# Kernel tuning notes

Hardware: AMD Instinct MI355X
Metric: run time of the kernel (lower is better)

Reference implementation:

```python
import jax, jax.numpy as jnp
import numpy as np

EMBED_DIM = 256
NUM_HEADS = 8
WINDOW = 64
HEAD_DIM = EMBED_DIM // NUM_HEADS


def setup_inputs() -> dict:
    key = jax.random.key(0)
    k_x, k_w, k_ow = jax.random.split(key, 3)
    B, S, E = 2, 4096, EMBED_DIM
    x = jax.random.normal(k_x, (B, S, E), dtype=jnp.float32)
    # nn.MultiheadAttention params: packed in_proj (q,k,v) and out_proj
    bound = 1.0 / np.sqrt(E)
    in_proj_w = jax.random.uniform(k_w, (3 * E, E), jnp.float32, -bound, bound)
    in_proj_b = jnp.zeros((3 * E,), jnp.float32)
    out_w = jax.random.uniform(k_ow, (E, E), jnp.float32, -bound, bound)
    out_b = jnp.zeros((E,), jnp.float32)
    return {"x": x, "in_proj_w": in_proj_w, "in_proj_b": in_proj_b,
            "out_w": out_w, "out_b": out_b}


def reference(x, in_proj_w, in_proj_b, out_w, out_b):
    B, S, E = x.shape
    H, D = NUM_HEADS, HEAD_DIM
    # packed qkv projection (torch Linear: y = x @ W^T + b)
    qkv = jnp.einsum('bse,fe->bsf', x, in_proj_w) + in_proj_b  # [B,S,3E]
    q, k, v = jnp.split(qkv, 3, axis=-1)
    q = q.reshape(B, S, H, D).transpose(0, 2, 1, 3)  # [B,H,S,D]
    k = k.reshape(B, S, H, D).transpose(0, 2, 1, 3)
    v = v.reshape(B, S, H, D).transpose(0, 2, 1, 3)
    scale = 1.0 / jnp.sqrt(jnp.asarray(D, x.dtype))
    scores = jnp.einsum('bhqd,bhkd->bhqk', q * scale, k)  # [B,H,S,S]
    idx = jnp.arange(S)
    band = jnp.abs(idx[:, None] - idx[None, :]) <= WINDOW  # [S,S]
    neg = jnp.asarray(-1e9, scores.dtype)
    scores = jnp.where(band[None, None, :, :], scores, neg)
    attn = jax.nn.softmax(scores, axis=-1)
    out = jnp.einsum('bhqk,bhkd->bhqd', attn, v)  # [B,H,S,D]
    out = out.transpose(0, 2, 1, 3).reshape(B, S, E)
    return jnp.einsum('bse,fe->bsf', out, out_w) + out_b
```

## Files before the change

### kernel.cpp

```cpp
#include <hip/hip_runtime.h>
#include <hip/hip_bf16.h>

#define S_LEN 4096
#define EMB   256
#define NHEAD 8
#define HDIM  32
#define WIN   64
#define BATCH 2

typedef __attribute__((ext_vector_type(8))) short short8;
typedef __attribute__((ext_vector_type(4))) float floatx4;
typedef unsigned short u16;
typedef unsigned int   u32;

static __device__ __forceinline__ u32 bf16_rn(float x) {
    u32 u = __float_as_uint(x);
    return (u + 0x7FFFu + ((u >> 16) & 1u)) >> 16;
}
static __device__ __forceinline__ u32 packsplit(float x) {
    const u32 hi = bf16_rn(x);
    const float hf = __uint_as_float(hi << 16);
    const u32 lo = bf16_rn(x - hf);
    return (hi << 16) | lo;
}
static __device__ __forceinline__ void unpack_pair(u32 p0, u32 p1, u32& h, u32& l) {
    h = (p0 >> 16) | (p1 & 0xFFFF0000u);
    l = (p0 & 0xFFFFu) | (p1 << 16);
}
static __device__ __forceinline__ void unpack8(uint4 a, uint4 b, uint4& h, uint4& l) {
    unpack_pair(a.x, a.y, h.x, l.x);
    unpack_pair(a.z, a.w, h.y, l.y);
    unpack_pair(b.x, b.y, h.z, l.z);
    unpack_pair(b.z, b.w, h.w, l.w);
}

#define NX4 524288
#define NW4 49152
#define NO4 16384

__global__ __launch_bounds__(256) void convert_kernel(
    const float* __restrict__ X, const float* __restrict__ Wi, const float* __restrict__ Wo,
    u32* __restrict__ Xp, u32* __restrict__ Wip, u32* __restrict__ Wop)
{
    const int i = blockIdx.x * 256 + threadIdx.x;
    const float* src; u32* dst; int off;
    if (i < NX4)            { src = X;  dst = Xp;  off = i; }
    else if (i < NX4 + NW4) { src = Wi; dst = Wip; off = i - NX4; }
    else                    { src = Wo; dst = Wop; off = i - NX4 - NW4; }
    const float4 v = *(const float4*)(src + (size_t)off * 4);
    uint4 o;
    o.x = packsplit(v.x); o.y = packsplit(v.y);
    o.z = packsplit(v.z); o.w = packsplit(v.w);
    *(uint4*)(dst + (size_t)off * 4) = o;
}

#define LDA 40

__global__ __launch_bounds__(256) void qkv_proj_kernel(
    const u32* __restrict__ Xp, const u32* __restrict__ Wp,
    const float* __restrict__ bias,
    u32* __restrict__ Qp, u32* __restrict__ Kp, u32* __restrict__ Vp)
{
    __shared__ __align__(16) u16 Ah[128 * LDA], Al[128 * LDA];
    __shared__ __align__(16) u16 Bh[64 * LDA],  Bl[64 * LDA];
    const int tid = threadIdx.x;
    const int m0 = blockIdx.y * 128, n0 = blockIdx.x * 64;
    const int srow = tid >> 2, sc = tid & 3;
    const int lane = tid & 63, wv = tid >> 6;
    const int wm = (wv >> 1) * 64, wn = (wv & 1) * 32;
    const int lm = lane & 15, kq = lane >> 4;

    uint4 pA[2][2], pB[2];
#pragma unroll
    for (int r = 0; r < 2; ++r) {
        const u32* base = Xp + (size_t)(m0 + srow + r * 64) * EMB + sc * 8;
        pA[r][0] = *(const uint4*)base;
        pA[r][1] = *(const uint4*)(base + 4);
    }
    {
        const u32* base = Wp + (size_t)(n0 + srow) * EMB + sc * 8;
        pB[0] = *(const uint4*)base;
        pB[1] = *(const uint4*)(base + 4);
    }

    floatx4 acc[4][2] = {};
    for (int t = 0; t < 8; ++t) {
        __syncthreads();
#pragma unroll
        for (int r = 0; r < 2; ++r) {
            uint4 h, l;
            unpack8(pA[r][0], pA[r][1], h, l);
            *(uint4*)&Ah[(srow + r * 64) * LDA + sc * 8] = h;
            *(uint4*)&Al[(srow + r * 64) * LDA + sc * 8] = l;
        }
        {
            uint4 h, l;
            unpack8(pB[0], pB[1], h, l);
            *(uint4*)&Bh[srow * LDA + sc * 8] = h;
            *(uint4*)&Bl[srow * LDA + sc * 8] = l;
        }
        __syncthreads();
        if (t < 7) {
            const int k0 = (t + 1) * 32;
#pragma unroll
            for (int r = 0; r < 2; ++r) {
                const u32* base = Xp + (size_t)(m0 + srow + r * 64) * EMB + k0 + sc * 8;
                pA[r][0] = *(const uint4*)base;
                pA[r][1] = *(const uint4*)(base + 4);
            }
            const u32* base = Wp + (size_t)(n0 + srow) * EMB + k0 + sc * 8;
            pB[0] = *(const uint4*)base;
            pB[1] = *(const uint4*)(base + 4);
        }
        short8 a_h[4], a_l[4], b_h[2], b_l[2];
#pragma unroll
        for (int mt = 0; mt < 4; ++mt) {
            a_h[mt] = *(const short8*)&Ah[(wm + mt * 16 + lm) * LDA + kq * 8];
            a_l[mt] = *(const short8*)&Al[(wm + mt * 16 + lm) * LDA + kq * 8];
        }
#pragma unroll
        for (int nt = 0; nt < 2; ++nt) {
            b_h[nt] = *(const short8*)&Bh[(wn + nt * 16 + lm) * LDA + kq * 8];
            b_l[nt] = *(const short8*)&Bl[(wn + nt * 16 + lm) * LDA + kq * 8];
        }
#pragma unroll
        for (int mt = 0; mt < 4; ++mt)
#pragma unroll
            for (int nt = 0; nt < 2; ++nt) {
                acc[mt][nt] = __builtin_amdgcn_mfma_f32_16x16x32_bf16(a_h[mt], b_h[nt], acc[mt][nt], 0, 0, 0);
                acc[mt][nt] = __builtin_amdgcn_mfma_f32_16x16x32_bf16(a_h[mt], b_l[nt], acc[mt][nt], 0, 0, 0);
                acc[mt][nt] = __builtin_amdgcn_mfma_f32_16x16x32_bf16(a_l[mt], b_h[nt], acc[mt][nt], 0, 0, 0);
            }
    }
#pragma unroll
    for (int nt = 0; nt < 2; ++nt) {
        const int f = n0 + wn + nt * 16 + lm;
        const int which = f >> 8;
        const int h = (f & 255) >> 5, d = f & 31;
        u32* dst = (which == 0) ? Qp : ((which == 1) ? Kp : Vp);
        const float sc2 = (which == 0) ? 0.17677669529663687f : 1.0f;
        const float bf = bias[f];
#pragma unroll
        for (int mt = 0; mt < 4; ++mt)
#pragma unroll
            for (int r = 0; r < 4; ++r) {
                const int m = m0 + wm + mt * 16 + kq * 4 + r;
                const int b = m >> 12, s = m & (S_LEN - 1);
                dst[(((size_t)b * NHEAD + h) * S_LEN + s) * HDIM + d]
                    = packsplit((acc[mt][nt][r] + bf) * sc2);
            }
    }
}

__global__ __launch_bounds__(256) void out_proj_kernel(
    const u32* __restrict__ Abp, const u32* __restrict__ Wp,
    const float* __restrict__ bias, float* __restrict__ C)
{
    __shared__ __align__(16) u16 Ah[128 * LDA], Al[128 * LDA];
    __shared__ __align__(16) u16 Bh[64 * LDA],  Bl[64 * LDA];
    const int tid = threadIdx.x;
    const int m0 = blockIdx.y * 128, n0 = blockIdx.x * 64;
    const int srow = tid >> 2, sc = tid & 3;
    const int lane = tid & 63, wv = tid >> 6;
    const int wm = (wv >> 1) * 64, wn = (wv & 1) * 32;
    const int lm = lane & 15, kq = lane >> 4;

    uint4 pA[2][2], pB[2];
#pragma unroll
    for (int r = 0; r < 2; ++r) {
        const u32* base = Abp + (size_t)(m0 + srow + r * 64) * EMB + sc * 8;
        pA[r][0] = *(const uint4*)base;
        pA[r][1] = *(const uint4*)(base + 4);
    }
    {
        const u32* base = Wp + (size_t)(n0 + srow) * EMB + sc * 8;
        pB[0] = *(const uint4*)base;
        pB[1] = *(const uint4*)(base + 4);
    }

    floatx4 acc[4][2] = {};
    for (int t = 0; t < 8; ++t) {
        __syncthreads();
#pragma unroll
        for (int r = 0; r < 2; ++r) {
            uint4 h, l;
            unpack8(pA[r][0], pA[r][1], h, l);
            *(uint4*)&Ah[(srow + r * 64) * LDA + sc * 8] = h;
            *(uint4*)&Al[(srow + r * 64) * LDA + sc * 8] = l;
        }
        {
            uint4 h, l;
            unpack8(pB[0], pB[1], h, l);
            *(uint4*)&Bh[srow * LDA + sc * 8] = h;
            *(uint4*)&Bl[srow * LDA + sc * 8] = l;
        }
        __syncthreads();
        if (t < 7) {
            const int k0 = (t + 1) * 32;
#pragma unroll
            for (int r = 0; r < 2; ++r) {
                const u32* base = Abp + (size_t)(m0 + srow + r * 64) * EMB + k0 + sc * 8;
                pA[r][0] = *(const uint4*)base;
                pA[r][1] = *(const uint4*)(base + 4);
            }
            const u32* base = Wp + (size_t)(n0 + srow) * EMB + k0 + sc * 8;
            pB[0] = *(const uint4*)base;
            pB[1] = *(const uint4*)(base + 4);
        }
        short8 a_h[4], a_l[4], b_h[2], b_l[2];
#pragma unroll
        for (int mt = 0; mt < 4; ++mt) {
            a_h[mt] = *(const short8*)&Ah[(wm + mt * 16 + lm) * LDA + kq * 8];
            a_l[mt] = *(const short8*)&Al[(wm + mt * 16 + lm) * LDA + kq * 8];
        }
#pragma unroll
        for (int nt = 0; nt < 2; ++nt) {
            b_h[nt] = *(const short8*)&Bh[(wn + nt * 16 + lm) * LDA + kq * 8];
            b_l[nt] = *(const short8*)&Bl[(wn + nt * 16 + lm) * LDA + kq * 8];
        }
#pragma unroll
        for (int mt = 0; mt < 4; ++mt)
#pragma unroll
            for (int nt = 0; nt < 2; ++nt) {
                acc[mt][nt] = __builtin_amdgcn_mfma_f32_16x16x32_bf16(a_h[mt], b_h[nt], acc[mt][nt], 0, 0, 0);
                acc[mt][nt] = __builtin_amdgcn_mfma_f32_16x16x32_bf16(a_h[mt], b_l[nt], acc[mt][nt], 0, 0, 0);
                acc[mt][nt] = __builtin_amdgcn_mfma_f32_16x16x32_bf16(a_l[mt], b_h[nt], acc[mt][nt], 0, 0, 0);
            }
    }
#pragma unroll
    for (int nt = 0; nt < 2; ++nt) {
        const int f = n0 + wn + nt * 16 + lm;
        const float bf = bias[f];
#pragma unroll
        for (int mt = 0; mt < 4; ++mt)
#pragma unroll
            for (int r = 0; r < 4; ++r) {
                const int m = m0 + wm + mt * 16 + kq * 4 + r;
                C[(size_t)m * EMB + f] = acc[mt][nt][r] + bf;
            }
    }
}

#define AKS 40
#define AVS 200
#define APS 200

__global__ __launch_bounds__(256) void local_attn_kernel(
    const u32* __restrict__ Qp, const u32* __restrict__ Kp,
    const u32* __restrict__ Vp, u32* __restrict__ Abp)
{
    __shared__ __align__(16) u16 Qh[64 * AKS], Ql[64 * AKS];
    __shared__ __align__(16) u16 Kh[192 * AKS], Kl[192 * AKS];
    __shared__ __align__(16) u16 Vt[32 * AVS];
    __shared__ __align__(16) u16 Pw[4 * 16 * APS];

    const int tid = threadIdx.x;
    const int q0 = blockIdx.x * 64;
    const int h = blockIdx.y, b = blockIdx.z;
    const int jmin = max(0, q0 - WIN);
    const int jmax = min(S_LEN - 1, q0 + 63 + WIN);
    const int nk = jmax - jmin + 1;
    const size_t bhS = ((size_t)b * NHEAD + h) * S_LEN;
    const size_t qoff = (bhS + q0) * HDIM;
    const size_t koff = (bhS + jmin) * HDIM;

    const int srow = tid >> 2, sc = tid & 3;
    {
        const u32* base = Qp + qoff + (size_t)srow * HDIM + sc * 8;
        uint4 h4, l4;
        unpack8(*(const uint4*)base, *(const uint4*)(base + 4), h4, l4);
        *(uint4*)&Qh[srow * AKS + sc * 8] = h4;
        *(uint4*)&Ql[srow * AKS + sc * 8] = l4;
    }
#pragma unroll
    for (int r = 0; r < 3; ++r) {
        const int t = srow + r * 64;
        const int tc = min(t, nk - 1);
        const u32* base = Kp + koff + (size_t)tc * HDIM + sc * 8;
        uint4 h4, l4;
        unpack8(*(const uint4*)base, *(const uint4*)(base + 4), h4, l4);
        *(uint4*)&Kh[t * AKS + sc * 8] = h4;
        *(uint4*)&Kl[t * AKS + sc * 8] = l4;
    }
#pragma unroll
    for (int r = 0; r < 3; ++r) {
        const int t = srow + r * 64;
        const int tc = min(t, nk - 1);
        const u32* base = Vp + koff + (size_t)tc * HDIM + sc * 8;
        const uint4 v0 = *(const uint4*)base;
        const uint4 v1 = *(const uint4*)(base + 4);
        const int d0 = sc * 8;
        Vt[(d0 + 0) * AVS + t] = (u16)(v0.x >> 16);
        Vt[(d0 + 1) * AVS + t] = (u16)(v0.y >> 16);
        Vt[(d0 + 2) * AVS + t] = (u16)(v0.z >> 16);
        Vt[(d0 + 3) * AVS + t] = (u16)(v0.w >> 16);
        Vt[(d0 + 4) * AVS + t] = (u16)(v1.x >> 16);
        Vt[(d0 + 5) * AVS + t] = (u16)(v1.y >> 16);
        Vt[(d0 + 6) * AVS + t] = (u16)(v1.z >> 16);
        Vt[(d0 + 7) * AVS + t] = (u16)(v1.w >> 16);
    }
    __syncthreads();

    const int lane = tid & 63, wv = tid >> 6;
    const int lm = lane & 15, quad = lane >> 4;
    const int qbase = wv * 16;

    const short8 qh = *(const short8*)&Qh[(qbase + lm) * AKS + quad * 8];
    const short8 ql = *(const short8*)&Ql[(qbase + lm) * AKS + quad * 8];

    floatx4 sacc[12];
#pragma unroll
    for (int nt = 0; nt < 12; ++nt) {
        const short8 bh = *(const short8*)&Kh[(nt * 16 + lm) * AKS + quad * 8];
        const short8 bl = *(const short8*)&Kl[(nt * 16 + lm) * AKS + quad * 8];
        floatx4 a = {};
        a = __builtin_amdgcn_mfma_f32_16x16x32_bf16(qh, bh, a, 0, 0, 0);
        a = __builtin_amdgcn_mfma_f32_16x16x32_bf16(qh, bl, a, 0, 0, 0);
        a = __builtin_amdgcn_mfma_f32_16x16x32_bf16(ql, bh, a, 0, 0, 0);
        sacc[nt] = a;
    }

    const int qg = q0 + qbase + quad * 4;
    float mx[4] = {-1e30f, -1e30f, -1e30f, -1e30f};
#pragma unroll
    for (int nt = 0; nt < 12; ++nt) {
        const int slot = nt * 16 + lm;
        const int keyg = jmin + slot;
#pragma unroll
        for (int r = 0; r < 4; ++r) {
            const int qr = qg + r;
            const bool valid = (slot < nk) && (keyg >= qr - WIN) && (keyg <= qr + WIN);
            const float sv = valid ? sacc[nt][r] : -1e30f;
            sacc[nt][r] = sv;
            mx[r] = fmaxf(mx[r], sv);
        }
    }
#pragma unroll
    for (int r = 0; r < 4; ++r) {
        mx[r] = fmaxf(mx[r], __shfl_xor(mx[r], 1));
        mx[r] = fmaxf(mx[r], __shfl_xor(mx[r], 2));
        mx[r] = fmaxf(mx[r], __shfl_xor(mx[r], 4));
        mx[r] = fmaxf(mx[r], __shfl_xor(mx[r], 8));
    }
    float l[4] = {0.f, 0.f, 0.f, 0.f};
    u16* Pme = &Pw[wv * 16 * APS];
#pragma unroll
    for (int nt = 0; nt < 12; ++nt)
#pragma unroll
        for (int r = 0; r < 4; ++r) {
            const float p = __expf(sacc[nt][r] - mx[r]);
            l[r] += p;
            Pme[(quad * 4 + r) * APS + nt * 16 + lm] = (u16)bf16_rn(p);
        }
#pragma unroll
    for (int r = 0; r < 4; ++r) {
        l[r] += __shfl_xor(l[r], 1);
        l[r] += __shfl_xor(l[r], 2);
        l[r] += __shfl_xor(l[r], 4);
        l[r] += __shfl_xor(l[r], 8);
    }
    const float rl[4] = {1.f / l[0], 1.f / l[1], 1.f / l[2], 1.f / l[3]};

    floatx4 oacc[2] = {};
#pragma unroll
    for (int ks = 0; ks < 6; ++ks) {
        const short8 ap  = *(const short8*)&Pme[lm * APS + ks * 32 + quad * 8];
        const short8 bv0 = *(const short8*)&Vt[lm * AVS + ks * 32 + quad * 8];
        const short8 bv1 = *(const short8*)&Vt[(16 + lm) * AVS + ks * 32 + quad * 8];
        oacc[0] = __builtin_amdgcn_mfma_f32_16x16x32_bf16(ap, bv0, oacc[0], 0, 0, 0);
        oacc[1] = __builtin_amdgcn_mfma_f32_16x16x32_bf16(ap, bv1, oacc[1], 0, 0, 0);
    }
#pragma unroll
    for (int nt = 0; nt < 2; ++nt)
#pragma unroll
        for (int r = 0; r < 4; ++r) {
            const int qrow = qbase + quad * 4 + r;
            Abp[((size_t)b * S_LEN + q0 + qrow) * EMB + h * HDIM + nt * 16 + lm]
                = packsplit(oacc[nt][r] * rl[r]);
        }
}

extern "C" void kernel_launch(void* const* d_in, const int* in_sizes, int n_in,
                              void* d_out, int out_size, void* d_ws, size_t ws_size,
                              hipStream_t stream) {
    const float* x  = (const float*)d_in[0];
    const float* wi = (const float*)d_in[1];
    const float* bi = (const float*)d_in[2];
    const float* wo = (const float*)d_in[3];
    const float* bo = (const float*)d_in[4];
    float* out = (float*)d_out;

    const size_t per = (size_t)BATCH * NHEAD * S_LEN * HDIM;
    u32* p = (u32*)d_ws;
    u32* Xp  = p; p += per;
    u32* Wip = p; p += 768 * EMB;
    u32* Wop = p; p += EMB * EMB;
    u32* Qp  = p; p += per;
    u32* Kp  = p; p += per;
    u32* Vp  = p; p += per;
    u32* Abp = p; p += per;

    convert_kernel<<<dim3((NX4 + NW4 + NO4) / 256), 256, 0, stream>>>(
        x, wi, wo, Xp, Wip, Wop);
    qkv_proj_kernel<<<dim3(768 / 64, 8192 / 128), 256, 0, stream>>>(
        Xp, Wip, bi, Qp, Kp, Vp);
    local_attn_kernel<<<dim3(S_LEN / 64, NHEAD, BATCH), 256, 0, stream>>>(
        Qp, Kp, Vp, Abp);
    out_proj_kernel<<<dim3(256 / 64, 8192 / 128), 256, 0, stream>>>(
        Abp, Wop, bo, out);
}
```

Measured before the change: 115.1 us.

## Compute transposed scores in registers and skip empty key tiles in local attention

The attention kernel now computes S^T (key-major) so each lane holds one query's scores. Q is loaded straight into registers and P is packed into MFMA A-operands without the shared-memory round trip. Each wave processes only the 10 key tiles that can overlap its band instead of all 12, which cuts MFMA work and LDS traffic. The output projection tile is also halved to 64 rows, doubling the grid to raise occupancy and parallelism, at the cost of less operand reuse per block.

```diff
diff --git a/kernel.cpp b/kernel.cpp
--- a/kernel.cpp
+++ b/kernel.cpp
@@ -156,21 +156,20 @@
     const u32* __restrict__ Abp, const u32* __restrict__ Wp,
     const float* __restrict__ bias, float* __restrict__ C)
 {
-    __shared__ __align__(16) u16 Ah[128 * LDA], Al[128 * LDA];
-    __shared__ __align__(16) u16 Bh[64 * LDA],  Bl[64 * LDA];
+    __shared__ __align__(16) u16 Ah[64 * LDA], Al[64 * LDA];
+    __shared__ __align__(16) u16 Bh[64 * LDA], Bl[64 * LDA];
     const int tid = threadIdx.x;
-    const int m0 = blockIdx.y * 128, n0 = blockIdx.x * 64;
+    const int m0 = blockIdx.y * 64, n0 = blockIdx.x * 64;
     const int srow = tid >> 2, sc = tid & 3;
     const int lane = tid & 63, wv = tid >> 6;
-    const int wm = (wv >> 1) * 64, wn = (wv & 1) * 32;
+    const int wm = (wv >> 1) * 32, wn = (wv & 1) * 32;
     const int lm = lane & 15, kq = lane >> 4;
 
-    uint4 pA[2][2], pB[2];
-#pragma unroll
-    for (int r = 0; r < 2; ++r) {
-        const u32* base = Abp + (size_t)(m0 + srow + r * 64) * EMB + sc * 8;
-        pA[r][0] = *(const uint4*)base;
-        pA[r][1] = *(const uint4*)(base + 4);
+    uint4 pA[2], pB[2];
+    {
+        const u32* base = Abp + (size_t)(m0 + srow) * EMB + sc * 8;
+        pA[0] = *(const uint4*)base;
+        pA[1] = *(const uint4*)(base + 4);
     }
     {
         const u32* base = Wp + (size_t)(n0 + srow) * EMB + sc * 8;
@@ -178,15 +177,14 @@
         pB[1] = *(const uint4*)(base + 4);
     }
 
-    floatx4 acc[4][2] = {};
+    floatx4 acc[2][2] = {};
     for (int t = 0; t < 8; ++t) {
         __syncthreads();
-#pragma unroll
-        for (int r = 0; r < 2; ++r) {
+        {
             uint4 h, l;
-            unpack8(pA[r][0], pA[r][1], h, l);
-            *(uint4*)&Ah[(srow + r * 64) * LDA + sc * 8] = h;
-            *(uint4*)&Al[(srow + r * 64) * LDA + sc * 8] = l;
+            unpack8(pA[0], pA[1], h, l);
+            *(uint4*)&Ah[srow * LDA + sc * 8] = h;
+            *(uint4*)&Al[srow * LDA + sc * 8] = l;
         }
         {
             uint4 h, l;
@@ -197,19 +195,18 @@
         __syncthreads();
         if (t < 7) {
             const int k0 = (t + 1) * 32;
-#pragma unroll
-            for (int r = 0; r < 2; ++r) {
-                const u32* base = Abp + (size_t)(m0 + srow + r * 64) * EMB + k0 + sc * 8;
-                pA[r][0] = *(const uint4*)base;
-                pA[r][1] = *(const uint4*)(base + 4);
+            {
+                const u32* base = Abp + (size_t)(m0 + srow) * EMB + k0 + sc * 8;
+                pA[0] = *(const uint4*)base;
+                pA[1] = *(const uint4*)(base + 4);
             }
             const u32* base = Wp + (size_t)(n0 + srow) * EMB + k0 + sc * 8;
             pB[0] = *(const uint4*)base;
             pB[1] = *(const uint4*)(base + 4);
         }
-        short8 a_h[4], a_l[4], b_h[2], b_l[2];
-#pragma unroll
-        for (int mt = 0; mt < 4; ++mt) {
+        short8 a_h[2], a_l[2], b_h[2], b_l[2];
+#pragma unroll
+        for (int mt = 0; mt < 2; ++mt) {
             a_h[mt] = *(const short8*)&Ah[(wm + mt * 16 + lm) * LDA + kq * 8];
             a_l[mt] = *(const short8*)&Al[(wm + mt * 16 + lm) * LDA + kq * 8];
         }
@@ -219,7 +216,7 @@
             b_l[nt] = *(const short8*)&Bl[(wn + nt * 16 + lm) * LDA + kq * 8];
         }
 #pragma unroll
-        for (int mt = 0; mt < 4; ++mt)
+        for (int mt = 0; mt < 2; ++mt)
 #pragma unroll
             for (int nt = 0; nt < 2; ++nt) {
                 acc[mt][nt] = __builtin_amdgcn_mfma_f32_16x16x32_bf16(a_h[mt], b_h[nt], acc[mt][nt], 0, 0, 0);
@@ -232,7 +229,7 @@
         const int f = n0 + wn + nt * 16 + lm;
         const float bf = bias[f];
 #pragma unroll
-        for (int mt = 0; mt < 4; ++mt)
+        for (int mt = 0; mt < 2; ++mt)
 #pragma unroll
             for (int r = 0; r < 4; ++r) {
                 const int m = m0 + wm + mt * 16 + kq * 4 + r;
@@ -243,16 +240,13 @@
 
 #define AKS 40
 #define AVS 200
-#define APS 200
 
 __global__ __launch_bounds__(256) void local_attn_kernel(
     const u32* __restrict__ Qp, const u32* __restrict__ Kp,
     const u32* __restrict__ Vp, u32* __restrict__ Abp)
 {
-    __shared__ __align__(16) u16 Qh[64 * AKS], Ql[64 * AKS];
     __shared__ __align__(16) u16 Kh[192 * AKS], Kl[192 * AKS];
     __shared__ __align__(16) u16 Vt[32 * AVS];
-    __shared__ __align__(16) u16 Pw[4 * 16 * APS];
 
     const int tid = threadIdx.x;
     const int q0 = blockIdx.x * 64;
@@ -264,14 +258,15 @@
     const size_t qoff = (bhS + q0) * HDIM;
     const size_t koff = (bhS + jmin) * HDIM;
 
+    const int lane = tid & 63, wv = tid >> 6;
+    const int lm = lane & 15, quad = lane >> 4;
+    const int qbase = wv * 16;
+
+    const u32* qb = Qp + qoff + (size_t)(qbase + lm) * HDIM + quad * 8;
+    const uint4 qp0 = *(const uint4*)qb;
+    const uint4 qp1 = *(const uint4*)(qb + 4);
+
     const int srow = tid >> 2, sc = tid & 3;
-    {
-        const u32* base = Qp + qoff + (size_t)srow * HDIM + sc * 8;
-        uint4 h4, l4;
-        unpack8(*(const uint4*)base, *(const uint4*)(base + 4), h4, l4);
-        *(uint4*)&Qh[srow * AKS + sc * 8] = h4;
-        *(uint4*)&Ql[srow * AKS + sc * 8] = l4;
-    }
 #pragma unroll
     for (int r = 0; r < 3; ++r) {
         const int t = srow + r * 64;
@@ -299,84 +294,100 @@
         Vt[(d0 + 6) * AVS + t] = (u16)(v1.z >> 16);
         Vt[(d0 + 7) * AVS + t] = (u16)(v1.w >> 16);
     }
+
+    short8 qh, ql;
+    {
+        uint4 h4, l4;
+        unpack8(qp0, qp1, h4, l4);
+        qh = *(const short8*)&h4;
+        ql = *(const short8*)&l4;
+    }
+
     __syncthreads();
 
-    const int lane = tid & 63, wv = tid >> 6;
-    const int lm = lane & 15, quad = lane >> 4;
-    const int qbase = wv * 16;
-
-    const short8 qh = *(const short8*)&Qh[(qbase + lm) * AKS + quad * 8];
-    const short8 ql = *(const short8*)&Ql[(qbase + lm) * AKS + quad * 8];
-
-    floatx4 sacc[12];
-#pragma unroll
-    for (int nt = 0; nt < 12; ++nt) {
-        const short8 bh = *(const short8*)&Kh[(nt * 16 + lm) * AKS + quad * 8];
-        const short8 bl = *(const short8*)&Kl[(nt * 16 + lm) * AKS + quad * 8];
+    const int tb = max(0, ((wv >> 1) << 1) + (min(q0 - WIN, 0) >> 4));
+
+    floatx4 sacc[10];
+#pragma unroll
+    for (int i = 0; i < 10; ++i) {
+        const int nt = tb + i;
+        const short8 kh = *(const short8*)&Kh[(nt * 16 + lm) * AKS + quad * 8];
+        const short8 kl = *(const short8*)&Kl[(nt * 16 + lm) * AKS + quad * 8];
         floatx4 a = {};
-        a = __builtin_amdgcn_mfma_f32_16x16x32_bf16(qh, bh, a, 0, 0, 0);
-        a = __builtin_amdgcn_mfma_f32_16x16x32_bf16(qh, bl, a, 0, 0, 0);
-        a = __builtin_amdgcn_mfma_f32_16x16x32_bf16(ql, bh, a, 0, 0, 0);
-        sacc[nt] = a;
-    }
-
-    const int qg = q0 + qbase + quad * 4;
-    float mx[4] = {-1e30f, -1e30f, -1e30f, -1e30f};
-#pragma unroll
-    for (int nt = 0; nt < 12; ++nt) {
-        const int slot = nt * 16 + lm;
-        const int keyg = jmin + slot;
+        a = __builtin_amdgcn_mfma_f32_16x16x32_bf16(kh, qh, a, 0, 0, 0);
+        a = __builtin_amdgcn_mfma_f32_16x16x32_bf16(kh, ql, a, 0, 0, 0);
+        a = __builtin_amdgcn_mfma_f32_16x16x32_bf16(kl, qh, a, 0, 0, 0);
+        sacc[i] = a;
+    }
+
+    const int qr = q0 + qbase + lm;
+    float mx = -1e30f;
+#pragma unroll
+    for (int i = 0; i < 10; ++i) {
+        const int sbase = (tb + i) * 16 + quad * 4;
 #pragma unroll
         for (int r = 0; r < 4; ++r) {
-            const int qr = qg + r;
+            const int slot = sbase + r;
+            const int keyg = jmin + slot;
             const bool valid = (slot < nk) && (keyg >= qr - WIN) && (keyg <= qr + WIN);
-            const float sv = valid ? sacc[nt][r] : -1e30f;
-            sacc[nt][r] = sv;
-            mx[r] = fmaxf(mx[r], sv);
-        }
-    }
-#pragma unroll
-    for (int r = 0; r < 4; ++r) {
-        mx[r] = fmaxf(mx[r], __shfl_xor(mx[r], 1));
-        mx[r] = fmaxf(mx[r], __shfl_xor(mx[r], 2));
-        mx[r] = fmaxf(mx[r], __shfl_xor(mx[r], 4));
-        mx[r] = fmaxf(mx[r], __shfl_xor(mx[r], 8));
-    }
-    float l[4] = {0.f, 0.f, 0.f, 0.f};
-    u16* Pme = &Pw[wv * 16 * APS];
-#pragma unroll
-    for (int nt = 0; nt < 12; ++nt)
-#pragma unroll
-        for (int r = 0; r < 4; ++r) {
-            const float p = __expf(sacc[nt][r] - mx[r]);
-            l[r] += p;
-            Pme[(quad * 4 + r) * APS + nt * 16 + lm] = (u16)bf16_rn(p);
-        }
-#pragma unroll
-    for (int r = 0; r < 4; ++r) {
-        l[r] += __shfl_xor(l[r], 1);
-        l[r] += __shfl_xor(l[r], 2);
-        l[r] += __shfl_xor(l[r], 4);
-        l[r] += __shfl_xor(l[r], 8);
-    }
-    const float rl[4] = {1.f / l[0], 1.f / l[1], 1.f / l[2], 1.f / l[3]};
-
+            const float sv = valid ? sacc[i][r] : -1e30f;
+            sacc[i][r] = sv;
+            mx = fmaxf(mx, sv);
+        }
+    }
+    mx = fmaxf(mx, __shfl_xor(mx, 16));
+    mx = fmaxf(mx, __shfl_xor(mx, 32));
+
+    float l = 0.f;
+    u32 pk_[20];
+#pragma unroll
+    for (int i = 0; i < 10; ++i) {
+        const float p0 = __expf(sacc[i][0] - mx);
+        const float p1 = __expf(sacc[i][1] - mx);
+        const float p2 = __expf(sacc[i][2] - mx);
+        const float p3 = __expf(sacc[i][3] - mx);
+        l += (p0 + p1) + (p2 + p3);
+        pk_[2 * i]     = bf16_rn(p0) | (bf16_rn(p1) << 16);
+        pk_[2 * i + 1] = bf16_rn(p2) | (bf16_rn(p3) << 16);
+    }
+    l += __shfl_xor(l, 16);
+    l += __shfl_xor(l, 32);
+    const float rl = 1.f / l;
+
+    const int kb = tb >> 1;
     floatx4 oacc[2] = {};
 #pragma unroll
-    for (int ks = 0; ks < 6; ++ks) {
-        const short8 ap  = *(const short8*)&Pme[lm * APS + ks * 32 + quad * 8];
-        const short8 bv0 = *(const short8*)&Vt[lm * AVS + ks * 32 + quad * 8];
-        const short8 bv1 = *(const short8*)&Vt[(16 + lm) * AVS + ks * 32 + quad * 8];
+    for (int i = 0; i < 5; ++i) {
+        const int ks = kb + i;
+        uint4 aw;
+        aw.x = pk_[4 * i + 0];
+        aw.y = pk_[4 * i + 1];
+        aw.z = pk_[4 * i + 2];
+        aw.w = pk_[4 * i + 3];
+        const short8 ap = *(const short8*)&aw;
+        const int sb = ks * 32 + quad * 4;
+        const uint2 e0 = *(const uint2*)&Vt[lm * AVS + sb];
+        const uint2 o0 = *(const uint2*)&Vt[lm * AVS + sb + 16];
+        const uint2 e1 = *(const uint2*)&Vt[(16 + lm) * AVS + sb];
+        const uint2 o1 = *(const uint2*)&Vt[(16 + lm) * AVS + sb + 16];
+        uint4 bw0; bw0.x = e0.x; bw0.y = e0.y; bw0.z = o0.x; bw0.w = o0.y;
+        uint4 bw1; bw1.x = e1.x; bw1.y = e1.y; bw1.z = o1.x; bw1.w = o1.y;
+        const short8 bv0 = *(const short8*)&bw0;
+        const short8 bv1 = *(const short8*)&bw1;
         oacc[0] = __builtin_amdgcn_mfma_f32_16x16x32_bf16(ap, bv0, oacc[0], 0, 0, 0);
         oacc[1] = __builtin_amdgcn_mfma_f32_16x16x32_bf16(ap, bv1, oacc[1], 0, 0, 0);
     }
+
+    float rlr[4];
+#pragma unroll
+    for (int r = 0; r < 4; ++r) rlr[r] = __shfl(rl, quad * 4 + r);
 #pragma unroll
     for (int nt = 0; nt < 2; ++nt)
 #pragma unroll
         for (int r = 0; r < 4; ++r) {
             const int qrow = qbase + quad * 4 + r;
             Abp[((size_t)b * S_LEN + q0 + qrow) * EMB + h * HDIM + nt * 16 + lm]
-                = packsplit(oacc[nt][r] * rl[r]);
+                = packsplit(oacc[nt][r] * rlr[r]);
         }
 }
 
@@ -406,6 +417,6 @@
         Xp, Wip, bi, Qp, Kp, Vp);
     local_attn_kernel<<<dim3(S_LEN / 64, NHEAD, BATCH), 256, 0, stream>>>(
         Qp, Kp, Vp, Abp);
-    out_proj_kernel<<<dim3(256 / 64, 8192 / 128), 256, 0, stream>>>(
+    out_proj_kernel<<<dim3(256 / 64, 8192 / 64), 256, 0, stream>>>(
         Abp, Wop, bo, out);
 }
```

New measurement: 110.9 us. 1.04x faster.
